# Optimization experiments

Hardware: AMD Instinct MI355X
Metric: run time of the kernel (lower is better)

## Reference

```python
import jax, jax.numpy as jnp
import numpy as np
from jax import lax

N = 16384          # total nodes
NUM_GRAPHS = 256   # graphs in the batch
K = 50             # self.knn
NUM_BINS = 5       # num_edge_features
RDF_CUTOFF = 10.0  # Angstrom-scale cutoff for Gaussian RDF smearing
BIG = 1e10         # masked-distance sentinel (finite, jit-safe)


def setup_inputs() -> dict:
    key = jax.random.key(0)
    k1, k2 = jax.random.split(key)
    # 3D pharmacophore coordinates, ~Angstrom scale
    pos = jax.random.normal(k1, (N, 3), dtype=jnp.float32) * 3.0
    # sorted graph-id vector (PyG `batch`)
    batch = jnp.sort(jax.random.randint(k2, (N,), 0, NUM_GRAPHS, dtype=jnp.int64))
    return {"pos": pos, "batch": batch}


def reference(pos, batch):
    n = pos.shape[0]
    # --- brute-force KNN graph (T.KNNGraph, per-graph via batch mask) ---
    sq = jnp.sum(pos * pos, axis=-1)                         # [n]
    d2 = sq[:, None] + sq[None, :] - 2.0 * (pos @ pos.T)     # [n, n]
    same_graph = batch[:, None] == batch[None, :]
    valid = same_graph & ~jnp.eye(n, dtype=bool)             # no self-loops
    d2m = jnp.where(valid, d2, BIG)
    neg_d2, nbr_idx = lax.top_k(-d2m, K)                     # [n, K] nearest by distance
    # symmetric-superset edge list: j -> i (source_to_target flow)
    src = nbr_idx.reshape(-1)                                # [n*K]
    dst = jnp.repeat(jnp.arange(n), K)                       # [n*K]
    edge_index = jnp.stack([src, dst])                       # [2, n*K]
    # --- T.Distance(norm=False): raw Euclidean edge lengths ---
    dist = jnp.sqrt(jnp.maximum(-neg_d2, 1e-12)).reshape(-1)  # [n*K]
    # --- DistanceRDF(num_bins): Gaussian smearing of distances over bins ---
    centers = jnp.linspace(0.0, RDF_CUTOFF, NUM_BINS, dtype=pos.dtype)
    spacing = RDF_CUTOFF / (NUM_BINS - 1)
    gamma = 1.0 / (2.0 * spacing * spacing)
    rdf = jnp.exp(-gamma * (dist[:, None] - centers[None, :]) ** 2)  # [n*K, NUM_BINS]
    return edge_index, dist, rdf
```

## Files before the change

### kernel.cpp

```cpp
#include <hip/hip_runtime.h>
#include <math.h>

#define NTOT  16384
#define NGR   256
#define KNN   50
#define NBINS 5
#define BIGF  1e10f
#define MAXJ  2

__global__ __launch_bounds__(256, 8)
void knn_fused(const float* __restrict__ pos,
               const int*   __restrict__ batch,
               float*       __restrict__ out)
{
    __shared__ unsigned int hish[4][128];
    __shared__ float        outst[4][352];

    const int i    = __builtin_amdgcn_readfirstlane((int)(blockIdx.x * 4 + (threadIdx.x >> 6)));
    const int wv   = threadIdx.x >> 6;
    const int lane = threadIdx.x & 63;

    const int g = batch[i];

    const int jA = i - 128 + lane;
    const int jB = i -  64 + lane;
    const int jC = i +   1 + lane;
    const int jD = i +  65 + lane;
    const int bA = batch[max(jA, 0)];
    const int bB = batch[max(jB, 0)];
    const int bC = batch[min(jC, NTOT - 1)];
    const int bD = batch[min(jD, NTOT - 1)];
    const int c_lo = __popcll(__ballot(jA >= 0 && bA == g))
                   + __popcll(__ballot(jB >= 0 && bB == g));
    const int c_hi = __popcll(__ballot(jC < NTOT && bC == g))
                   + __popcll(__ballot(jD < NTOT && bD == g));
    const int start = i - c_lo;
    const int end   = i + 1 + c_hi;
    const int cnt   = end - start;
    const int J     = (cnt + 63) >> 6;

    const float xi = pos[(size_t)i * 3 + 0];
    const float yi = pos[(size_t)i * 3 + 1];
    const float zi = pos[(size_t)i * 3 + 2];
    const float sqi = xi * xi + yi * yi + zi * zi;

    unsigned int hi[MAXJ];
    bool valid[MAXJ];
    #pragma unroll
    for (int j = 0; j < MAXJ; ++j) {
        const int c = j * 64 + lane;
        valid[j] = (j < J) && (c < cnt) && ((start + c) != i);
        float d2 = BIGF;
        if (valid[j]) {
            const int idx = start + c;
            const float xj = pos[(size_t)idx * 3 + 0];
            const float yj = pos[(size_t)idx * 3 + 1];
            const float zj = pos[(size_t)idx * 3 + 2];
            const float sqj = xj * xj + yj * yj + zj * zj;
            const float dot = xi * xj + yi * yj + zi * zj;
            d2 = sqi + sqj - 2.0f * dot;
        }
        const unsigned int b = __float_as_uint(d2);
        hi[j] = ((int)b < 0) ? ~b : (b | 0x80000000u);
        hish[wv][c] = hi[j];
    }

    int rank[MAXJ] = {0, 0};
    const int kpad = (cnt + 7) & ~7;
    const uint4* __restrict__ k4 = reinterpret_cast<const uint4*>(&hish[wv][0]);
    if (J == 1) {
        int ra = 0, rb = 0;
        for (int c0 = 0; c0 < kpad; c0 += 8) {
            const uint4 A = k4[(c0 >> 2) + 0];
            const uint4 B = k4[(c0 >> 2) + 1];
            ra += (A.x < hi[0]) + (A.y < hi[0]) + (A.z < hi[0]) + (A.w < hi[0]);
            rb += (B.x < hi[0]) + (B.y < hi[0]) + (B.z < hi[0]) + (B.w < hi[0]);
        }
        rank[0] = ra + rb;
    } else {
        int ra0 = 0, rb0 = 0, ra1 = 0, rb1 = 0;
        for (int c0 = 0; c0 < kpad; c0 += 8) {
            const uint4 A = k4[(c0 >> 2) + 0];
            const uint4 B = k4[(c0 >> 2) + 1];
            ra0 += (A.x < hi[0]) + (A.y < hi[0]) + (A.z < hi[0]) + (A.w < hi[0]);
            rb0 += (B.x < hi[0]) + (B.y < hi[0]) + (B.z < hi[0]) + (B.w < hi[0]);
            ra1 += (A.x < hi[1]) + (A.y < hi[1]) + (A.z < hi[1]) + (A.w < hi[1]);
            rb1 += (B.x < hi[1]) + (B.y < hi[1]) + (B.z < hi[1]) + (B.w < hi[1]);
        }
        rank[0] = ra0 + rb0;
        rank[1] = ra1 + rb1;
    }

    {
        int s = (valid[0] ? rank[0] : 0) + (valid[1] ? rank[1] : 0);
        #pragma unroll
        for (int off = 32; off > 0; off >>= 1) s += __shfl_xor(s, off, 64);
        const int expect = ((cnt - 1) * (cnt - 2)) >> 1;
        if (s != expect) {
            #pragma unroll
            for (int j = 0; j < MAXJ; ++j) {
                if (!valid[j]) continue;
                const int c = j * 64 + lane;
                int r = 0;
                for (int k = 0; k < cnt; ++k) {
                    const unsigned int h = hish[wv][k];
                    r += (h < hi[j]) || (h == hi[j] && k < c);
                }
                rank[j] = r;
            }
        }
    }

    const float centers[NBINS] = {0.0f, 2.5f, 5.0f, 7.5f, 10.0f};
    const float gamma = 0.08f;
    const float fi = (float)i;

    #pragma unroll
    for (int j = 0; j < MAXJ; ++j) {
        const int c = j * 64 + lane;
        if (valid[j] && rank[j] < KNN) {
            const unsigned int s  = hi[j];
            const unsigned int b  = (s & 0x80000000u) ? (s & 0x7fffffffu) : ~s;
            const float d2 = __uint_as_float(b);
            const float d  = sqrtf(fmaxf(d2, 1e-12f));
            const int   r  = rank[j];
            outst[wv][r]        = (float)(start + c);
            outst[wv][50 + r]   = d;
            #pragma unroll
            for (int bb = 0; bb < NBINS; ++bb) {
                const float dd = d - centers[bb];
                outst[wv][100 + r * NBINS + bb] = __expf(-gamma * dd * dd);
            }
        }
    }
    if (cnt <= KNN) {
        const int r = (cnt - 1) + lane;
        if (r < KNN) {
            const int m = lane;
            int jj;
            if (m < start)       jj = m;
            else if (m == start) jj = i;
            else                 jj = end + (m - start - 1);
            outst[wv][r]      = (float)jj;
            outst[wv][50 + r] = 100000.0f;
            #pragma unroll
            for (int bb = 0; bb < NBINS; ++bb)
                outst[wv][100 + r * NBINS + bb] = 0.0f;
        }
    }

    float* __restrict__ srcO  = out;
    float* __restrict__ dstO  = out + (size_t)NTOT * KNN;
    float* __restrict__ distO = out + (size_t)2 * NTOT * KNN;
    float* __restrict__ rdfO  = out + (size_t)3 * NTOT * KNN;

    const size_t eb = (size_t)i * KNN;
    if (lane < KNN) {
        srcO [eb + lane] = outst[wv][lane];
        dstO [eb + lane] = fi;
        distO[eb + lane] = outst[wv][50 + lane];
    }
    float* __restrict__ rbase = rdfO + (size_t)i * (KNN * NBINS);
    #pragma unroll
    for (int q = 0; q < 4; ++q) {
        const int idx = lane + 64 * q;
        if (idx < KNN * NBINS)
            rbase[idx] = outst[wv][100 + idx];
    }
}

extern "C" void kernel_launch(void* const* d_in, const int* in_sizes, int n_in,
                              void* d_out, int out_size, void* d_ws, size_t ws_size,
                              hipStream_t stream) {
    const float* pos   = (const float*)d_in[0];
    const int*   batch = (const int*)d_in[1];
    float*       out   = (float*)d_out;

    knn_fused<<<dim3(NTOT / 4), dim3(256), 0, stream>>>(pos, batch, out);
}
```

Baseline: 75.22 us.

## Process two query nodes per wavefront, sharing batch scan and candidate loads

Each wavefront now handles two consecutive nodes. It does one combined batch-window scan, and when both nodes are in the same graph it computes both distance rows from a single load of the candidate positions. The grid is halved, so the per-wave cost of segment discovery and position fetches is amortized over two nodes. In exchange each wave carries more registers, LDS use doubles and the occupancy hint drops to 4, and the different-graph case falls back to processing the two nodes one after the other.

```diff
diff --git a/kernel.cpp b/kernel.cpp
--- a/kernel.cpp
+++ b/kernel.cpp
@@ -2,50 +2,88 @@
 #include <math.h>
 
 #define NTOT  16384
-#define NGR   256
 #define KNN   50
 #define NBINS 5
 #define BIGF  1e10f
 #define MAXJ  2
 
-__global__ __launch_bounds__(256, 8)
-void knn_fused(const float* __restrict__ pos,
-               const int*   __restrict__ batch,
-               float*       __restrict__ out)
-{
-    __shared__ unsigned int hish[4][128];
-    __shared__ float        outst[4][352];
-
-    const int i    = __builtin_amdgcn_readfirstlane((int)(blockIdx.x * 4 + (threadIdx.x >> 6)));
-    const int wv   = threadIdx.x >> 6;
-    const int lane = threadIdx.x & 63;
-
-    const int g = batch[i];
-
-    const int jA = i - 128 + lane;
-    const int jB = i -  64 + lane;
-    const int jC = i +   1 + lane;
-    const int jD = i +  65 + lane;
-    const int bA = batch[max(jA, 0)];
-    const int bB = batch[max(jB, 0)];
-    const int bC = batch[min(jC, NTOT - 1)];
-    const int bD = batch[min(jD, NTOT - 1)];
-    const int c_lo = __popcll(__ballot(jA >= 0 && bA == g))
-                   + __popcll(__ballot(jB >= 0 && bB == g));
-    const int c_hi = __popcll(__ballot(jC < NTOT && bC == g))
-                   + __popcll(__ballot(jD < NTOT && bD == g));
-    const int start = i - c_lo;
-    const int end   = i + 1 + c_hi;
-    const int cnt   = end - start;
-    const int J     = (cnt + 63) >> 6;
-
+
+__device__ __forceinline__ unsigned int sortable_u32(float d2)
+{
+    const unsigned int b = __float_as_uint(d2);
+    return ((int)b < 0) ? ~b : (b | 0x80000000u);
+}
+
+__device__ __forceinline__ float unsortable_f32(unsigned int s)
+{
+    const unsigned int b = (s & 0x80000000u) ? (s & 0x7fffffffu) : ~s;
+    return __uint_as_float(b);
+}
+
+__device__ __forceinline__ void stage_and_flush(
+    float* __restrict__ out, float* __restrict__ stg,
+    const unsigned int (&hi)[MAXJ], const bool (&valid)[MAXJ],
+    const int (&rank)[MAXJ], int i, int start, int cnt, int lane)
+{
+    const float centers[NBINS] = {0.0f, 2.5f, 5.0f, 7.5f, 10.0f};
+    const float gamma = 0.08f;
+    #pragma unroll
+    for (int j = 0; j < MAXJ; ++j) {
+        if (valid[j] && rank[j] < KNN) {
+            const int c = j * 64 + lane;
+            const float d = sqrtf(fmaxf(unsortable_f32(hi[j]), 1e-12f));
+            const int r = rank[j];
+            stg[r]      = (float)(start + c);
+            stg[50 + r] = d;
+            #pragma unroll
+            for (int bb = 0; bb < NBINS; ++bb) {
+                const float dd = d - centers[bb];
+                stg[100 + r * NBINS + bb] = __expf(-gamma * dd * dd);
+            }
+        }
+    }
+    if (cnt <= KNN) {
+        const int r = (cnt - 1) + lane;
+        if (r < KNN) {
+            const int m = lane;
+            int jj;
+            if (m < start)       jj = m;
+            else if (m == start) jj = i;
+            else                 jj = (start + cnt) + (m - start - 1);
+            stg[r]      = (float)jj;
+            stg[50 + r] = 100000.0f;
+            #pragma unroll
+            for (int bb = 0; bb < NBINS; ++bb)
+                stg[100 + r * NBINS + bb] = 0.0f;
+        }
+    }
+    const size_t eb = (size_t)i * KNN;
+    if (lane < KNN) {
+        out[eb + lane]                          = stg[lane];
+        out[(size_t)NTOT * KNN + eb + lane]     = (float)i;
+        out[(size_t)2 * NTOT * KNN + eb + lane] = stg[50 + lane];
+    }
+    float* __restrict__ rbase = out + (size_t)3 * NTOT * KNN + (size_t)i * (KNN * NBINS);
+    #pragma unroll
+    for (int q = 0; q < 4; ++q) {
+        const int idx = lane + 64 * q;
+        if (idx < KNN * NBINS)
+            rbase[idx] = stg[100 + idx];
+    }
+}
+
+__device__ __forceinline__ void one_node(
+    const float* __restrict__ pos, float* __restrict__ out,
+    int i, int start, int cnt, int lane,
+    unsigned int* __restrict__ keyl, float* __restrict__ stg)
+{
+    const int J = (cnt + 63) >> 6;
     const float xi = pos[(size_t)i * 3 + 0];
     const float yi = pos[(size_t)i * 3 + 1];
     const float zi = pos[(size_t)i * 3 + 2];
     const float sqi = xi * xi + yi * yi + zi * zi;
 
-    unsigned int hi[MAXJ];
-    bool valid[MAXJ];
+    unsigned int hi[MAXJ]; bool valid[MAXJ];
     #pragma unroll
     for (int j = 0; j < MAXJ; ++j) {
         const int c = j * 64 + lane;
@@ -60,112 +98,180 @@
             const float dot = xi * xj + yi * yj + zi * zj;
             d2 = sqi + sqj - 2.0f * dot;
         }
-        const unsigned int b = __float_as_uint(d2);
-        hi[j] = ((int)b < 0) ? ~b : (b | 0x80000000u);
-        hish[wv][c] = hi[j];
+        hi[j] = sortable_u32(d2);
+        keyl[c] = hi[j];
     }
 
     int rank[MAXJ] = {0, 0};
     const int kpad = (cnt + 7) & ~7;
-    const uint4* __restrict__ k4 = reinterpret_cast<const uint4*>(&hish[wv][0]);
-    if (J == 1) {
-        int ra = 0, rb = 0;
-        for (int c0 = 0; c0 < kpad; c0 += 8) {
-            const uint4 A = k4[(c0 >> 2) + 0];
-            const uint4 B = k4[(c0 >> 2) + 1];
-            ra += (A.x < hi[0]) + (A.y < hi[0]) + (A.z < hi[0]) + (A.w < hi[0]);
-            rb += (B.x < hi[0]) + (B.y < hi[0]) + (B.z < hi[0]) + (B.w < hi[0]);
-        }
-        rank[0] = ra + rb;
-    } else {
-        int ra0 = 0, rb0 = 0, ra1 = 0, rb1 = 0;
-        for (int c0 = 0; c0 < kpad; c0 += 8) {
-            const uint4 A = k4[(c0 >> 2) + 0];
-            const uint4 B = k4[(c0 >> 2) + 1];
-            ra0 += (A.x < hi[0]) + (A.y < hi[0]) + (A.z < hi[0]) + (A.w < hi[0]);
-            rb0 += (B.x < hi[0]) + (B.y < hi[0]) + (B.z < hi[0]) + (B.w < hi[0]);
-            ra1 += (A.x < hi[1]) + (A.y < hi[1]) + (A.z < hi[1]) + (A.w < hi[1]);
-            rb1 += (B.x < hi[1]) + (B.y < hi[1]) + (B.z < hi[1]) + (B.w < hi[1]);
-        }
-        rank[0] = ra0 + rb0;
-        rank[1] = ra1 + rb1;
+    const uint4* __restrict__ k4 = reinterpret_cast<const uint4*>(keyl);
+    for (int c0 = 0; c0 < kpad; c0 += 8) {
+        const uint4 A = k4[(c0 >> 2) + 0];
+        const uint4 B = k4[(c0 >> 2) + 1];
+        #pragma unroll
+        for (int j = 0; j < MAXJ; ++j) {
+            rank[j] += (A.x < hi[j]) + (A.y < hi[j]) + (A.z < hi[j]) + (A.w < hi[j])
+                     + (B.x < hi[j]) + (B.y < hi[j]) + (B.z < hi[j]) + (B.w < hi[j]);
+        }
     }
 
     {
         int s = (valid[0] ? rank[0] : 0) + (valid[1] ? rank[1] : 0);
         #pragma unroll
         for (int off = 32; off > 0; off >>= 1) s += __shfl_xor(s, off, 64);
-        const int expect = ((cnt - 1) * (cnt - 2)) >> 1;
-        if (s != expect) {
+        if (s != (((cnt - 1) * (cnt - 2)) >> 1)) {
             #pragma unroll
             for (int j = 0; j < MAXJ; ++j) {
                 if (!valid[j]) continue;
                 const int c = j * 64 + lane;
                 int r = 0;
                 for (int k = 0; k < cnt; ++k) {
-                    const unsigned int h = hish[wv][k];
+                    const unsigned int h = keyl[k];
                     r += (h < hi[j]) || (h == hi[j] && k < c);
                 }
                 rank[j] = r;
             }
         }
     }
-
-    const float centers[NBINS] = {0.0f, 2.5f, 5.0f, 7.5f, 10.0f};
-    const float gamma = 0.08f;
-    const float fi = (float)i;
-
-    #pragma unroll
-    for (int j = 0; j < MAXJ; ++j) {
-        const int c = j * 64 + lane;
-        if (valid[j] && rank[j] < KNN) {
-            const unsigned int s  = hi[j];
-            const unsigned int b  = (s & 0x80000000u) ? (s & 0x7fffffffu) : ~s;
-            const float d2 = __uint_as_float(b);
-            const float d  = sqrtf(fmaxf(d2, 1e-12f));
-            const int   r  = rank[j];
-            outst[wv][r]        = (float)(start + c);
-            outst[wv][50 + r]   = d;
-            #pragma unroll
-            for (int bb = 0; bb < NBINS; ++bb) {
-                const float dd = d - centers[bb];
-                outst[wv][100 + r * NBINS + bb] = __expf(-gamma * dd * dd);
-            }
-        }
-    }
-    if (cnt <= KNN) {
-        const int r = (cnt - 1) + lane;
-        if (r < KNN) {
-            const int m = lane;
-            int jj;
-            if (m < start)       jj = m;
-            else if (m == start) jj = i;
-            else                 jj = end + (m - start - 1);
-            outst[wv][r]      = (float)jj;
-            outst[wv][50 + r] = 100000.0f;
-            #pragma unroll
-            for (int bb = 0; bb < NBINS; ++bb)
-                outst[wv][100 + r * NBINS + bb] = 0.0f;
-        }
-    }
-
-    float* __restrict__ srcO  = out;
-    float* __restrict__ dstO  = out + (size_t)NTOT * KNN;
-    float* __restrict__ distO = out + (size_t)2 * NTOT * KNN;
-    float* __restrict__ rdfO  = out + (size_t)3 * NTOT * KNN;
-
-    const size_t eb = (size_t)i * KNN;
-    if (lane < KNN) {
-        srcO [eb + lane] = outst[wv][lane];
-        dstO [eb + lane] = fi;
-        distO[eb + lane] = outst[wv][50 + lane];
-    }
-    float* __restrict__ rbase = rdfO + (size_t)i * (KNN * NBINS);
+    stage_and_flush(out, stg, hi, valid, rank, i, start, cnt, lane);
+}
+
+__global__ __launch_bounds__(256, 4)
+void knn_fused2(const float* __restrict__ pos,
+                const int*   __restrict__ batch,
+                float*       __restrict__ out)
+{
+    __shared__ unsigned int keys[4][2][128];
+    __shared__ float        stg [4][2][352];
+
+    const int w    = __builtin_amdgcn_readfirstlane((int)(blockIdx.x * 4 + (threadIdx.x >> 6)));
+    const int wv   = threadIdx.x >> 6;
+    const int lane = threadIdx.x & 63;
+    const int i0 = 2 * w, i1 = i0 + 1;
+
+    const int g0 = batch[i0];
+    const int g1 = batch[i1];
+
+    const int base = i0 - 127;
+    int wq[4]; bool ir[4];
     #pragma unroll
     for (int q = 0; q < 4; ++q) {
-        const int idx = lane + 64 * q;
-        if (idx < KNN * NBINS)
-            rbase[idx] = outst[wv][100 + idx];
+        const int j = base + lane + 64 * q;
+        ir[q] = (j >= 0) && (j < NTOT);
+        wq[q] = batch[min(max(j, 0), NTOT - 1)];
+    }
+    const unsigned long long m00 = __ballot(ir[0] && wq[0] == g0);
+    const unsigned long long m01 = __ballot(ir[1] && wq[1] == g0);
+    const unsigned long long m02 = __ballot(ir[2] && wq[2] == g0);
+    const unsigned long long m03 = __ballot(ir[3] && wq[3] == g0);
+    const int c_lo0 = __popcll(m00) + __popcll(m01 & ~(1ull << 63));
+    const int c_hi0 = __popcll(m02) + __popcll(m03);
+    const int start0 = i0 - c_lo0;
+    const int cnt0   = c_lo0 + 1 + c_hi0;
+
+    if (g0 == g1) {
+        const int S = start0, C = cnt0;
+        const int J = (C + 63) >> 6;
+
+        const float x0 = pos[(size_t)i0 * 3 + 0], y0 = pos[(size_t)i0 * 3 + 1], z0 = pos[(size_t)i0 * 3 + 2];
+        const float x1 = pos[(size_t)i1 * 3 + 0], y1 = pos[(size_t)i1 * 3 + 1], z1 = pos[(size_t)i1 * 3 + 2];
+        const float sq0 = x0 * x0 + y0 * y0 + z0 * z0;
+        const float sq1 = x1 * x1 + y1 * y1 + z1 * z1;
+
+        unsigned int h0[MAXJ], h1[MAXJ];
+        bool v0[MAXJ], v1[MAXJ];
+        #pragma unroll
+        for (int j = 0; j < MAXJ; ++j) {
+            const int c = j * 64 + lane;
+            const bool inb = (j < J) && (c < C);
+            const int idx = S + c;
+            v0[j] = inb && (idx != i0);
+            v1[j] = inb && (idx != i1);
+            float d20 = BIGF, d21 = BIGF;
+            if (inb) {
+                const float xj = pos[(size_t)idx * 3 + 0];
+                const float yj = pos[(size_t)idx * 3 + 1];
+                const float zj = pos[(size_t)idx * 3 + 2];
+                const float sqj = xj * xj + yj * yj + zj * zj;
+                if (idx != i0) d20 = sq0 + sqj - 2.0f * (x0 * xj + y0 * yj + z0 * zj);
+                if (idx != i1) d21 = sq1 + sqj - 2.0f * (x1 * xj + y1 * yj + z1 * zj);
+            }
+            h0[j] = sortable_u32(d20);  keys[wv][0][c] = h0[j];
+            h1[j] = sortable_u32(d21);  keys[wv][1][c] = h1[j];
+        }
+
+        int r0[MAXJ] = {0, 0}, r1[MAXJ] = {0, 0};
+        const int kpad = (C + 7) & ~7;
+        const uint4* __restrict__ k40 = reinterpret_cast<const uint4*>(&keys[wv][0][0]);
+        const uint4* __restrict__ k41 = reinterpret_cast<const uint4*>(&keys[wv][1][0]);
+        if (J == 1) {
+            int a0 = 0, b0 = 0, a1 = 0, b1 = 0;
+            for (int c0 = 0; c0 < kpad; c0 += 8) {
+                const uint4 A0 = k40[(c0 >> 2) + 0], B0 = k40[(c0 >> 2) + 1];
+                const uint4 A1 = k41[(c0 >> 2) + 0], B1 = k41[(c0 >> 2) + 1];
+                a0 += (A0.x < h0[0]) + (A0.y < h0[0]) + (A0.z < h0[0]) + (A0.w < h0[0]);
+                b0 += (B0.x < h0[0]) + (B0.y < h0[0]) + (B0.z < h0[0]) + (B0.w < h0[0]);
+                a1 += (A1.x < h1[0]) + (A1.y < h1[0]) + (A1.z < h1[0]) + (A1.w < h1[0]);
+                b1 += (B1.x < h1[0]) + (B1.y < h1[0]) + (B1.z < h1[0]) + (B1.w < h1[0]);
+            }
+            r0[0] = a0 + b0;  r1[0] = a1 + b1;
+        } else {
+            for (int c0 = 0; c0 < kpad; c0 += 8) {
+                const uint4 A0 = k40[(c0 >> 2) + 0], B0 = k40[(c0 >> 2) + 1];
+                const uint4 A1 = k41[(c0 >> 2) + 0], B1 = k41[(c0 >> 2) + 1];
+                #pragma unroll
+                for (int j = 0; j < MAXJ; ++j) {
+                    r0[j] += (A0.x < h0[j]) + (A0.y < h0[j]) + (A0.z < h0[j]) + (A0.w < h0[j])
+                           + (B0.x < h0[j]) + (B0.y < h0[j]) + (B0.z < h0[j]) + (B0.w < h0[j]);
+                    r1[j] += (A1.x < h1[j]) + (A1.y < h1[j]) + (A1.z < h1[j]) + (A1.w < h1[j])
+                           + (B1.x < h1[j]) + (B1.y < h1[j]) + (B1.z < h1[j]) + (B1.w < h1[j]);
+                }
+            }
+        }
+
+        {
+            int s = (v0[0] ? r0[0] : 0) + (v0[1] ? r0[1] : 0)
+                  + (v1[0] ? r1[0] : 0) + (v1[1] ? r1[1] : 0);
+            #pragma unroll
+            for (int off = 32; off > 0; off >>= 1) s += __shfl_xor(s, off, 64);
+            if (s != ((C - 1) * (C - 2))) {
+                #pragma unroll
+                for (int j = 0; j < MAXJ; ++j) {
+                    const int c = j * 64 + lane;
+                    if (v0[j]) {
+                        int r = 0;
+                        for (int k = 0; k < C; ++k) {
+                            const unsigned int h = keys[wv][0][k];
+                            r += (h < h0[j]) || (h == h0[j] && k < c);
+                        }
+                        r0[j] = r;
+                    }
+                    if (v1[j]) {
+                        int r = 0;
+                        for (int k = 0; k < C; ++k) {
+                            const unsigned int h = keys[wv][1][k];
+                            r += (h < h1[j]) || (h == h1[j] && k < c);
+                        }
+                        r1[j] = r;
+                    }
+                }
+            }
+        }
+
+        stage_and_flush(out, &stg[wv][0][0], h0, v0, r0, i0, S, C, lane);
+        stage_and_flush(out, &stg[wv][1][0], h1, v1, r1, i1, S, C, lane);
+    } else {
+        const unsigned long long m10 = __ballot(ir[0] && wq[0] == g1);
+        const unsigned long long m11 = __ballot(ir[1] && wq[1] == g1);
+        const unsigned long long m12 = __ballot(ir[2] && wq[2] == g1);
+        const unsigned long long m13 = __ballot(ir[3] && wq[3] == g1);
+        const int c_lo1 = __popcll(m10) + __popcll(m11);
+        const int c_hi1 = __popcll(m12 & ~1ull) + __popcll(m13);
+        const int start1 = i1 - c_lo1;
+        const int cnt1   = c_lo1 + 1 + c_hi1;
+
+        one_node(pos, out, i0, start0, cnt0, lane, &keys[wv][0][0], &stg[wv][0][0]);
+        one_node(pos, out, i1, start1, cnt1, lane, &keys[wv][1][0], &stg[wv][1][0]);
     }
 }
 
@@ -176,5 +282,5 @@
     const int*   batch = (const int*)d_in[1];
     float*       out   = (float*)d_out;
 
-    knn_fused<<<dim3(NTOT / 4), dim3(256), 0, stream>>>(pos, batch, out);
-}
+    knn_fused2<<<dim3(NTOT / 8), dim3(256), 0, stream>>>(pos, batch, out);
+}
```

After: 75.62 us. No clear change (+0.5%).
